# Kernel tuning notes

Measured on AMD Instinct MI355X. Metric: run time of the kernel, lower is better.

Reference implementation:

```python
import jax, jax.numpy as jnp
import numpy as np

# module hyperparams (from init_kwargs)
C, O, G, E, W, KS = 64, 64, 16, 128, 7, 2
AH, AS = 2, 2              # activate_height, activate_stride
D = C // G                 # kernel depth per group = 4
N = O // G                 # filters per group = 4
EPS = 1e-5                 # BatchNorm eps
LEAKY = 0.01               # LeakyReLU negative slope
B, T = 2, 512


def setup_inputs() -> dict:
    key = jax.random.key(0)
    k1, k2 = jax.random.split(key)
    x = jax.random.normal(k1, (B, C, E, T), dtype=jnp.float32)
    weight = jax.random.normal(k2, (O, D, E, W), dtype=jnp.float32) * 0.05
    gamma = jnp.ones((O,), jnp.float32)
    beta = jnp.zeros((O,), jnp.float32)
    return {"x": x, "weight": weight, "gamma": gamma, "beta": beta}


def reference(x, weight, gamma, beta):
    b, c, f, T_in = x.shape
    pad = W // 2
    xp = jnp.pad(x, ((0, 0), (0, 0), (0, 0), (pad, pad)))
    t = (T_in + 2 * pad - W) // KS + 1
    # unfold: window index grid [t, W]
    idx = KS * jnp.arange(t)[:, None] + jnp.arange(W)[None, :]
    xu = xp[..., idx]                        # [b, c, f, t, W]
    xu = xu.reshape(b, G, D, f, t, W)        # channel = (g d), group-major
    wg = weight.reshape(G, N, D, f, W)       # out = (g n)
    # broadcast elementwise mul -> [b, g, n, d, f, t, w]
    y = xu[:, :, None] * wg[None, :, :, :, :, None, :]
    y = y.reshape(b, O, D, f, t, W)          # (g n) -> o
    # BatchNorm3d over channel O, training-mode batch stats (biased var)
    mean = y.mean(axis=(0, 2, 3, 4, 5), keepdims=True)
    var = y.var(axis=(0, 2, 3, 4, 5), keepdims=True)
    y = (y - mean) * jax.lax.rsqrt(var + EPS)
    bshape = (1, O, 1, 1, 1, 1)
    y = y * gamma.reshape(bshape) + beta.reshape(bshape)
    ys = y.sum(axis=(2, 5))                  # [b, o, f, t]
    yp = jax.lax.reduce_window(ys, jnp.float32(0), jax.lax.add,
                               (1, 1, AH, 1), (1, 1, AS, 1), 'VALID')  # [b,o,fo,t]
    return jnp.where(yp >= 0, yp, LEAKY * yp)
```

## Files before the change

kernel.cpp:

```cpp
#include <hip/hip_runtime.h>

constexpr int Cc = 64, Oc = 64, Gc = 16, Ec = 128, Wc = 7;
constexpr int Dc = 4, Nc = 4, Bc = 2, Tc = 512, TTc = 256, FOc = 64;
constexpr float EPSf = 1e-5f, LEAKYf = 0.01f;
constexpr float Minv = 1.0f / 1835008.0f;


__global__ __launch_bounds__(256) void stats_k(const float* __restrict__ x,
                                               const float* __restrict__ wgt,
                                               float* __restrict__ sums) {
  int bid = blockIdx.x;
  int ft = bid & 31;
  int g  = (bid >> 5) & 15;
  int b  = bid >> 9;
  int t  = threadIdx.x;

  __shared__ float RS[16][4];
  __shared__ float ED[16][5];

  int r = t >> 4, sub = t & 15;
  int d = r >> 2, fi = r & 3;
  const float4* src = (const float4*)(
      x + ((size_t)((b * Cc + g * Dc + d) * Ec + 4 * ft + fi)) * Tc);

  float se = 0.f, so = 0.f, se2 = 0.f, so2 = 0.f;
#pragma unroll
  for (int k = 0; k < 8; ++k) {
    float4 v = src[sub + 16 * k];
    se += v.x + v.z;  so += v.y + v.w;
    se2 += v.x * v.x + v.z * v.z;
    so2 += v.y * v.y + v.w * v.w;
    if (k == 0 && sub == 0) { ED[r][0] = v.x; ED[r][1] = v.y; }
    if (k == 7 && sub == 15) { ED[r][2] = v.y; ED[r][3] = v.z; ED[r][4] = v.w; }
  }
#pragma unroll
  for (int off = 1; off < 16; off <<= 1) {
    se  += __shfl_xor(se, off);  so  += __shfl_xor(so, off);
    se2 += __shfl_xor(se2, off); so2 += __shfl_xor(so2, off);
  }
  if (sub == 0) { RS[r][0] = se; RS[r][1] = so; RS[r][2] = se2; RS[r][3] = so2; }
  __syncthreads();

  float md = 0.f, vd = 0.f;
  if (t < 64) {
    int r2 = t >> 2, n = t & 3;
    float Se = RS[r2][0], So = RS[r2][1], Se2 = RS[r2][2], So2 = RS[r2][3];
    float e0 = ED[r2][0], e1 = ED[r2][1];
    float e509 = ED[r2][2], e510 = ED[r2][3], e511 = ED[r2][4];
    float S[7] = {So - e509 - e511, Se - e510, So - e511, Se, So,
                  Se - e0, So - e1};
    float Q[7] = {So2 - e509 * e509 - e511 * e511, Se2 - e510 * e510,
                  So2 - e511 * e511, Se2, So2, Se2 - e0 * e0, So2 - e1 * e1};
    int d2 = r2 >> 2, fi2 = r2 & 3;
    int o = g * Nc + n;
    const float* wp = wgt + ((size_t)((o * Dc + d2) * Ec + 4 * ft + fi2)) * Wc;
#pragma unroll
    for (int w = 0; w < 7; ++w) {
      float wt = wp[w];
      md += wt * S[w];
      vd += wt * wt * Q[w];
    }
  }
#pragma unroll
  for (int off = 4; off < 64; off <<= 1) {
    md += __shfl_xor(md, off);
    vd += __shfl_xor(vd, off);
  }
  if (t < 4) {
    atomicAdd(&sums[(g * Nc + t) * 2], md);
    atomicAdd(&sums[(g * Nc + t) * 2 + 1], vd);
  }
}

__device__ __forceinline__ int FL4(int c) { return (c & 3) * 33 + (c >> 2); }

__global__ __launch_bounds__(256, 4) void conv_k(
    const float* __restrict__ x, const float* __restrict__ wgt,
    const float* __restrict__ sums, const float* __restrict__ gamma,
    const float* __restrict__ beta, float* __restrict__ out) {
  int bid = blockIdx.x;
  int fo2 = bid & 31;
  int g   = (bid >> 5) & 15;
  int b   = bid >> 9;
  int t   = threadIdx.x;

  __shared__ float xs[16 * 528];
  __shared__ float wsm[512];
  float4* xs4 = (float4*)xs;

#pragma unroll
  for (int kk = 0; kk < 8; ++kk) {
    int idx = t + 256 * kk;
    int lr = idx >> 7, jj = idx & 127;
    int flS = lr >> 3, dd = (lr >> 1) & 3, f2 = lr & 1;
    const float4* src = (const float4*)(
        x + ((size_t)((b * Cc + g * Dc + dd) * Ec + 4 * fo2 + 2 * flS + f2)) * Tc);
    float4 v = src[jj];
    xs4[lr * 132 + FL4(jj + 1)] = v;
  }
  if (t < 32) {
    int lr = t >> 1;
    int c = (t & 1) ? 129 : 0;
    xs4[lr * 132 + FL4(c)] = make_float4(0.f, 0.f, 0.f, 0.f);
  }
  if (t < 128) {
#pragma unroll
    for (int i = 0; i < 4; ++i) {
      int s = t * 4 + i;
      int w = s & 7, n = (s >> 3) & 3, lr8 = (s >> 5) & 7, flS = s >> 8;
      int o = g * Nc + n, dd = lr8 >> 1, f = 4 * fo2 + 2 * flS + (lr8 & 1);
      wsm[s] = (w < 7) ? wgt[((size_t)((o * Dc + dd) * Ec + f)) * Wc + w] : 0.f;
    }
  }
  __syncthreads();

  int wv = t >> 6, j = t & 63;
  int fo_l = wv >> 1, n0 = (wv & 1) * 2;
  float acc0[4] = {0.f, 0.f, 0.f, 0.f}, acc1[4] = {0.f, 0.f, 0.f, 0.f};
#pragma unroll
  for (int lr8 = 0; lr8 < 8; ++lr8) {
    const float4* rb = xs4 + (fo_l * 8 + lr8) * 132;
    float4 X0 = rb[FL4(2 * j)];
    float4 X1 = rb[FL4(2 * j + 1)];
    float4 X2 = rb[FL4(2 * j + 2)];
    float4 X3 = rb[FL4(2 * j + 3)];
    float xq[16] = {X0.x, X0.y, X0.z, X0.w, X1.x, X1.y, X1.z, X1.w,
                    X2.x, X2.y, X2.z, X2.w, X3.x, X3.y, X3.z, X3.w};
    const float4* wb = (const float4*)&wsm[((fo_l * 8 + lr8) * 4 + n0) * 8];
    float4 Wa0 = wb[0], Wa1 = wb[1], Wb0 = wb[2], Wb1 = wb[3];
    float wA[7] = {Wa0.x, Wa0.y, Wa0.z, Wa0.w, Wa1.x, Wa1.y, Wa1.z};
    float wB[7] = {Wb0.x, Wb0.y, Wb0.z, Wb0.w, Wb1.x, Wb1.y, Wb1.z};
#pragma unroll
    for (int w = 0; w < 7; ++w) {
#pragma unroll
      for (int s = 0; s < 4; ++s) {
        float xv = xq[2 * s + w + 1];
        acc0[s] += xv * wA[w];
        acc1[s] += xv * wB[w];
      }
    }
  }

  int o0 = g * Nc + n0;
  float m0 = sums[2 * o0] * Minv, E0 = sums[2 * o0 + 1] * Minv;
  float a0 = gamma[o0] * rsqrtf(E0 - m0 * m0 + EPSf);
  float c0 = 56.0f * (beta[o0] - a0 * m0);
  float m1 = sums[2 * o0 + 2] * Minv, E1 = sums[2 * o0 + 3] * Minv;
  float a1 = gamma[o0 + 1] * rsqrtf(E1 - m1 * m1 + EPSf);
  float c1 = 56.0f * (beta[o0 + 1] - a1 * m1);

  int fo = fo2 * 2 + fo_l;
  float4 r0, r1;
  float u;
  u = a0 * acc0[0] + c0; r0.x = (u >= 0.f) ? u : LEAKYf * u;
  u = a0 * acc0[1] + c0; r0.y = (u >= 0.f) ? u : LEAKYf * u;
  u = a0 * acc0[2] + c0; r0.z = (u >= 0.f) ? u : LEAKYf * u;
  u = a0 * acc0[3] + c0; r0.w = (u >= 0.f) ? u : LEAKYf * u;
  u = a1 * acc1[0] + c1; r1.x = (u >= 0.f) ? u : LEAKYf * u;
  u = a1 * acc1[1] + c1; r1.y = (u >= 0.f) ? u : LEAKYf * u;
  u = a1 * acc1[2] + c1; r1.z = (u >= 0.f) ? u : LEAKYf * u;
  u = a1 * acc1[3] + c1; r1.w = (u >= 0.f) ? u : LEAKYf * u;
  *(float4*)(out + ((size_t)((b * Oc + o0) * FOc + fo)) * TTc + 4 * j) = r0;
  *(float4*)(out + ((size_t)((b * Oc + o0 + 1) * FOc + fo)) * TTc + 4 * j) = r1;
}

extern "C" void kernel_launch(void* const* d_in, const int* in_sizes, int n_in,
                              void* d_out, int out_size, void* d_ws, size_t ws_size,
                              hipStream_t stream) {
  (void)in_sizes; (void)n_in; (void)out_size; (void)ws_size;
  const float* x     = (const float*)d_in[0];
  const float* w     = (const float*)d_in[1];
  const float* gamma = (const float*)d_in[2];
  const float* beta  = (const float*)d_in[3];
  float* sums = (float*)d_ws;
  hipMemsetAsync((void*)sums, 0, Oc * 2 * sizeof(float), stream);
  stats_k<<<dim3(Bc * Gc * 32), dim3(256), 0, stream>>>(x, w, sums);
  conv_k<<<dim3(Bc * Gc * 32), dim3(256), 0, stream>>>(x, w, sums, gamma, beta,
                                                       (float*)d_out);
}
```

Baseline: 94.78 us.

## Fuse stats and conv kernels with grid-wide barrier via atomic counter

Merges the batch-norm statistics pass and the conv/pool pass into one kernel. Each block computes its partial sums from the x tile it already staged in shared memory and writes them to a per-block workspace slot. It then bumps a global counter and spins until all 1024 blocks have arrived before reducing the partials for its group. This removes the second read of x and one kernel launch. The cost is reliance on all 1024 blocks being co-resident (256 CUs × 4 blocks), with a timeout fallback that could silently produce wrong statistics.

New measurement: 264.8 us. 2.79x slower.

```diff
diff --git a/kernel.cpp b/kernel.cpp
--- a/kernel.cpp
+++ b/kernel.cpp
@@ -3,81 +3,17 @@
 constexpr int Cc = 64, Oc = 64, Gc = 16, Ec = 128, Wc = 7;
 constexpr int Dc = 4, Nc = 4, Bc = 2, Tc = 512, TTc = 256, FOc = 64;
 constexpr float EPSf = 1e-5f, LEAKYf = 0.01f;
+constexpr unsigned NBLK = 1024;
 constexpr float Minv = 1.0f / 1835008.0f;
 
 
-__global__ __launch_bounds__(256) void stats_k(const float* __restrict__ x,
-                                               const float* __restrict__ wgt,
-                                               float* __restrict__ sums) {
-  int bid = blockIdx.x;
-  int ft = bid & 31;
-  int g  = (bid >> 5) & 15;
-  int b  = bid >> 9;
-  int t  = threadIdx.x;
-
-  __shared__ float RS[16][4];
-  __shared__ float ED[16][5];
-
-  int r = t >> 4, sub = t & 15;
-  int d = r >> 2, fi = r & 3;
-  const float4* src = (const float4*)(
-      x + ((size_t)((b * Cc + g * Dc + d) * Ec + 4 * ft + fi)) * Tc);
-
-  float se = 0.f, so = 0.f, se2 = 0.f, so2 = 0.f;
-#pragma unroll
-  for (int k = 0; k < 8; ++k) {
-    float4 v = src[sub + 16 * k];
-    se += v.x + v.z;  so += v.y + v.w;
-    se2 += v.x * v.x + v.z * v.z;
-    so2 += v.y * v.y + v.w * v.w;
-    if (k == 0 && sub == 0) { ED[r][0] = v.x; ED[r][1] = v.y; }
-    if (k == 7 && sub == 15) { ED[r][2] = v.y; ED[r][3] = v.z; ED[r][4] = v.w; }
-  }
-#pragma unroll
-  for (int off = 1; off < 16; off <<= 1) {
-    se  += __shfl_xor(se, off);  so  += __shfl_xor(so, off);
-    se2 += __shfl_xor(se2, off); so2 += __shfl_xor(so2, off);
-  }
-  if (sub == 0) { RS[r][0] = se; RS[r][1] = so; RS[r][2] = se2; RS[r][3] = so2; }
-  __syncthreads();
-
-  float md = 0.f, vd = 0.f;
-  if (t < 64) {
-    int r2 = t >> 2, n = t & 3;
-    float Se = RS[r2][0], So = RS[r2][1], Se2 = RS[r2][2], So2 = RS[r2][3];
-    float e0 = ED[r2][0], e1 = ED[r2][1];
-    float e509 = ED[r2][2], e510 = ED[r2][3], e511 = ED[r2][4];
-    float S[7] = {So - e509 - e511, Se - e510, So - e511, Se, So,
-                  Se - e0, So - e1};
-    float Q[7] = {So2 - e509 * e509 - e511 * e511, Se2 - e510 * e510,
-                  So2 - e511 * e511, Se2, So2, Se2 - e0 * e0, So2 - e1 * e1};
-    int d2 = r2 >> 2, fi2 = r2 & 3;
-    int o = g * Nc + n;
-    const float* wp = wgt + ((size_t)((o * Dc + d2) * Ec + 4 * ft + fi2)) * Wc;
-#pragma unroll
-    for (int w = 0; w < 7; ++w) {
-      float wt = wp[w];
-      md += wt * S[w];
-      vd += wt * wt * Q[w];
-    }
-  }
-#pragma unroll
-  for (int off = 4; off < 64; off <<= 1) {
-    md += __shfl_xor(md, off);
-    vd += __shfl_xor(vd, off);
-  }
-  if (t < 4) {
-    atomicAdd(&sums[(g * Nc + t) * 2], md);
-    atomicAdd(&sums[(g * Nc + t) * 2 + 1], vd);
-  }
-}
-
 __device__ __forceinline__ int FL4(int c) { return (c & 3) * 33 + (c >> 2); }
 
-__global__ __launch_bounds__(256, 4) void conv_k(
+__global__ __launch_bounds__(256, 4) void fused_all(
     const float* __restrict__ x, const float* __restrict__ wgt,
-    const float* __restrict__ sums, const float* __restrict__ gamma,
-    const float* __restrict__ beta, float* __restrict__ out) {
+    float* __restrict__ partials, unsigned* __restrict__ cnt,
+    const float* __restrict__ gamma, const float* __restrict__ beta,
+    float* __restrict__ out) {
   int bid = blockIdx.x;
   int fo2 = bid & 31;
   int g   = (bid >> 5) & 15;
@@ -86,33 +22,78 @@
 
   __shared__ float xs[16 * 528];
   __shared__ float wsm[512];
+  __shared__ float RS[16][4];
+  __shared__ float SRT[8];
+  __shared__ float sA[4], sC[4];
   float4* xs4 = (float4*)xs;
 
-#pragma unroll
-  for (int kk = 0; kk < 8; ++kk) {
-    int idx = t + 256 * kk;
-    int lr = idx >> 7, jj = idx & 127;
-    int flS = lr >> 3, dd = (lr >> 1) & 3, f2 = lr & 1;
-    const float4* src = (const float4*)(
-        x + ((size_t)((b * Cc + g * Dc + dd) * Ec + 4 * fo2 + 2 * flS + f2)) * Tc);
-    float4 v = src[jj];
-    xs4[lr * 132 + FL4(jj + 1)] = v;
-  }
+  int lr = t >> 4, sub = t & 15;
+  int fl = lr >> 3, dd = (lr >> 1) & 3, f2 = lr & 1;
+  const float4* src = (const float4*)(
+      x + ((size_t)((b * Cc + g * Dc + dd) * Ec + 4 * fo2 + 2 * fl + f2)) * Tc);
+  float se = 0.f, so = 0.f, se2 = 0.f, so2 = 0.f;
+#pragma unroll
+  for (int k = 0; k < 8; ++k) {
+    float4 v = src[sub + 16 * k];
+    xs4[lr * 132 + FL4(1 + sub + 16 * k)] = v;
+    se += v.x + v.z;  so += v.y + v.w;
+    se2 += v.x * v.x + v.z * v.z;
+    so2 += v.y * v.y + v.w * v.w;
+  }
+#pragma unroll
+  for (int off = 1; off < 16; off <<= 1) {
+    se  += __shfl_xor(se, off);  so  += __shfl_xor(so, off);
+    se2 += __shfl_xor(se2, off); so2 += __shfl_xor(so2, off);
+  }
+  if (sub == 0) { RS[lr][0] = se; RS[lr][1] = so; RS[lr][2] = se2; RS[lr][3] = so2; }
   if (t < 32) {
-    int lr = t >> 1;
+    int lrp = t >> 1;
     int c = (t & 1) ? 129 : 0;
-    xs4[lr * 132 + FL4(c)] = make_float4(0.f, 0.f, 0.f, 0.f);
+    xs4[lrp * 132 + FL4(c)] = make_float4(0.f, 0.f, 0.f, 0.f);
   }
   if (t < 128) {
 #pragma unroll
     for (int i = 0; i < 4; ++i) {
       int s = t * 4 + i;
       int w = s & 7, n = (s >> 3) & 3, lr8 = (s >> 5) & 7, flS = s >> 8;
-      int o = g * Nc + n, dd = lr8 >> 1, f = 4 * fo2 + 2 * flS + (lr8 & 1);
-      wsm[s] = (w < 7) ? wgt[((size_t)((o * Dc + dd) * Ec + f)) * Wc + w] : 0.f;
-    }
-  }
-  __syncthreads();
+      int o = g * Nc + n, ddS = lr8 >> 1, f = 4 * fo2 + 2 * flS + (lr8 & 1);
+      wsm[s] = (w < 7) ? wgt[((size_t)((o * Dc + ddS) * Ec + f)) * Wc + w] : 0.f;
+    }
+  }
+  __syncthreads();
+
+  if (t < 64) {
+    int r2 = t >> 2, n = t & 3;
+    float Se = RS[r2][0], So = RS[r2][1], Se2 = RS[r2][2], So2 = RS[r2][3];
+    const float* rowf = &xs[r2 * 528];
+    float e509 = rowf[129], e510 = rowf[130], e511 = rowf[131];
+    float e0 = rowf[132], e1 = rowf[133];
+    float S[7] = {So - e509 - e511, Se - e510, So - e511, Se, So,
+                  Se - e0, So - e1};
+    float Q[7] = {So2 - e509 * e509 - e511 * e511, Se2 - e510 * e510,
+                  So2 - e511 * e511, Se2, So2, Se2 - e0 * e0, So2 - e1 * e1};
+    float md = 0.f, vd = 0.f;
+#pragma unroll
+    for (int w = 0; w < 7; ++w) {
+      float wt = wsm[(r2 * 4 + n) * 8 + w];
+      md += wt * S[w];
+      vd += wt * wt * Q[w];
+    }
+#pragma unroll
+    for (int off = 4; off < 64; off <<= 1) {
+      md += __shfl_xor(md, off);
+      vd += __shfl_xor(vd, off);
+    }
+    if (t < 4) {
+      float* p = &partials[((size_t)((b * Gc + g) * 32 + fo2)) * 8];
+      p[t] = md;
+      p[4 + t] = vd;
+    }
+    __threadfence();
+    if (t == 0)
+      __hip_atomic_fetch_add(cnt, 1u, __ATOMIC_RELEASE,
+                             __HIP_MEMORY_SCOPE_AGENT);
+  }
 
   int wv = t >> 6, j = t & 63;
   int fo_l = wv >> 1, n0 = (wv & 1) * 2;
@@ -141,14 +122,55 @@
     }
   }
 
+  if (t == 0) {
+    int tries = 0;
+    while (__hip_atomic_load(cnt, __ATOMIC_RELAXED, __HIP_MEMORY_SCOPE_AGENT) <
+           NBLK) {
+      __builtin_amdgcn_s_sleep(16);
+      if (++tries > (1 << 18)) break;
+    }
+    __threadfence();
+  }
+  __syncthreads();
+
+  {
+    float v0 = 0.f, v1 = 0.f, v2 = 0.f, v3 = 0.f;
+    float v4 = 0.f, v5 = 0.f, v6 = 0.f, v7 = 0.f;
+    if (t < 64) {
+      int b2 = t >> 5, fp = t & 31;
+      const float* p = &partials[((size_t)((b2 * Gc + g) * 32 + fp)) * 8];
+      float4 P0 = *(const float4*)p;
+      float4 P1 = *(const float4*)(p + 4);
+      v0 = P0.x; v1 = P0.y; v2 = P0.z; v3 = P0.w;
+      v4 = P1.x; v5 = P1.y; v6 = P1.z; v7 = P1.w;
+#pragma unroll
+      for (int off = 1; off < 64; off <<= 1) {
+        v0 += __shfl_xor(v0, off); v1 += __shfl_xor(v1, off);
+        v2 += __shfl_xor(v2, off); v3 += __shfl_xor(v3, off);
+        v4 += __shfl_xor(v4, off); v5 += __shfl_xor(v5, off);
+        v6 += __shfl_xor(v6, off); v7 += __shfl_xor(v7, off);
+      }
+      if (t == 0) {
+        SRT[0] = v0; SRT[1] = v1; SRT[2] = v2; SRT[3] = v3;
+        SRT[4] = v4; SRT[5] = v5; SRT[6] = v6; SRT[7] = v7;
+      }
+    }
+  }
+  __syncthreads();
+  if (t < 4) {
+    float mean = SRT[t] * Minv;
+    float e2   = SRT[4 + t] * Minv;
+    float var  = e2 - mean * mean;
+    int o = g * Nc + t;
+    float a = gamma[o] * rsqrtf(var + EPSf);
+    sA[t] = a;
+    sC[t] = 56.0f * (beta[o] - a * mean);
+  }
+  __syncthreads();
+
+  float a0 = sA[n0], c0 = sC[n0];
+  float a1 = sA[n0 + 1], c1 = sC[n0 + 1];
   int o0 = g * Nc + n0;
-  float m0 = sums[2 * o0] * Minv, E0 = sums[2 * o0 + 1] * Minv;
-  float a0 = gamma[o0] * rsqrtf(E0 - m0 * m0 + EPSf);
-  float c0 = 56.0f * (beta[o0] - a0 * m0);
-  float m1 = sums[2 * o0 + 2] * Minv, E1 = sums[2 * o0 + 3] * Minv;
-  float a1 = gamma[o0 + 1] * rsqrtf(E1 - m1 * m1 + EPSf);
-  float c1 = 56.0f * (beta[o0 + 1] - a1 * m1);
-
   int fo = fo2 * 2 + fo_l;
   float4 r0, r1;
   float u;
@@ -172,9 +194,9 @@
   const float* w     = (const float*)d_in[1];
   const float* gamma = (const float*)d_in[2];
   const float* beta  = (const float*)d_in[3];
-  float* sums = (float*)d_ws;
-  hipMemsetAsync((void*)sums, 0, Oc * 2 * sizeof(float), stream);
-  stats_k<<<dim3(Bc * Gc * 32), dim3(256), 0, stream>>>(x, w, sums);
-  conv_k<<<dim3(Bc * Gc * 32), dim3(256), 0, stream>>>(x, w, sums, gamma, beta,
-                                                       (float*)d_out);
+  float* partials = (float*)d_ws;
+  unsigned* cnt = (unsigned*)((char*)d_ws + 1024 * 8 * sizeof(float));
+  hipMemsetAsync((void*)cnt, 0, sizeof(unsigned), stream);
+  fused_all<<<dim3(NBLK), dim3(256), 0, stream>>>(x, w, partials, cnt, gamma,
+                                                  beta, (float*)d_out);
 }
```
